# Kernel tuning notes

Hardware: AMD Instinct MI355X
Metric: run time of the kernel (lower is better)

## Reference

```python
import jax, jax.numpy as jnp
import numpy as np

DIM = 768
HEADS = 12
HEAD_DIM = DIM // HEADS
WS = 32                      # window_size (Wh == Ww)
N = WS * WS + 1              # tokens = patches + CLS
B = 8
NUM_REL = (2 * WS - 1) * (2 * WS - 1) + 3


def _rel_pos_index():
    # Mirrors the torch buffer construction (meshgrid indexing='ij').
    coords = np.stack(np.meshgrid(np.arange(WS), np.arange(WS), indexing='ij')).reshape(2, -1)
    rel = (coords[:, :, None] - coords[:, None, :]).transpose(1, 2, 0)  # [M, M, 2]
    rel[..., 0] += WS - 1
    rel[..., 1] += WS - 1
    rel[..., 0] *= 2 * WS - 1
    idx = np.zeros((N, N), dtype=np.int32)
    idx[1:, 1:] = rel.sum(-1)
    idx[0, :] = NUM_REL - 3
    idx[:, 0] = NUM_REL - 2
    idx[0, 0] = NUM_REL - 1
    return idx


def setup_inputs() -> dict:
    key = jax.random.key(0)
    ks = jax.random.split(key, 4)
    s = DIM ** -0.5
    return {
        "x": jax.random.normal(ks[0], (B, N, DIM), dtype=jnp.float32),
        "qkv_w": jax.random.normal(ks[1], (3 * DIM, DIM), dtype=jnp.float32) * s,
        "q_bias": jnp.zeros((DIM,), dtype=jnp.float32),
        "v_bias": jnp.zeros((DIM,), dtype=jnp.float32),
        "rpb_table": jax.random.normal(ks[2], (NUM_REL, HEADS), dtype=jnp.float32) * 0.02,
        "proj_w": jax.random.normal(ks[3], (DIM, DIM), dtype=jnp.float32) * s,
        "proj_b": jnp.zeros((DIM,), dtype=jnp.float32),
        "rel_pos_index": jnp.asarray(_rel_pos_index()),
    }


def reference(x, qkv_w, q_bias, v_bias, rpb_table, proj_w, proj_b, rel_pos_index):
    Bx, Nx, C = x.shape
    scale = HEAD_DIM ** -0.5
    # qkv bias = [q_bias, zeros, v_bias] (k has no bias)
    qkv_bias = jnp.concatenate([q_bias, jnp.zeros_like(v_bias), v_bias])
    qkv = x @ qkv_w.T + qkv_bias                           # [B, N, 3*C]
    qkv = qkv.reshape(Bx, Nx, 3, HEADS, HEAD_DIM).transpose(2, 0, 3, 1, 4)
    q, k, v = qkv[0] * scale, qkv[1], qkv[2]               # [B, H, N, d]
    attn = jnp.einsum('bhqd,bhkd->bhqk', q, k)             # [B, H, N, N]
    rpb = rpb_table[rel_pos_index]                         # [N, N, H] gather
    attn = attn + rpb.transpose(2, 0, 1)[None]             # broadcast over batch
    attn = jax.nn.softmax(attn, axis=-1)
    out = jnp.einsum('bhqk,bhkd->bhqd', attn, v)           # [B, H, N, d]
    out = out.transpose(0, 2, 1, 3).reshape(Bx, Nx, -1)    # [B, N, C]
    return out @ proj_w.T + proj_b
```

## Files before the change

kernel.cpp:

```cpp
#include <hip/hip_runtime.h>

typedef _Float16 f16;
typedef __attribute__((ext_vector_type(4))) _Float16 f16x4;
typedef __attribute__((ext_vector_type(8))) _Float16 f16x8;
typedef __attribute__((ext_vector_type(4))) float f32x4;

#define BATCH 8
#define NTOK 1025
#define DIM 768
#define HEADS 12
#define HD 64
#define MTOT (BATCH * NTOK)
#define MPAD 8320
#define NQP2 1152
#define NKP 1088
#define NUMREL 3972

#define DMA_FENCE asm volatile("s_waitcnt vmcnt(0)" ::: "memory")

__device__ __forceinline__ int imin(int a, int b) { return a < b ? a : b; }

__device__ __forceinline__ void gl_lds16(const f16* g, f16* l) {
  __builtin_amdgcn_global_load_lds(
      (const __attribute__((address_space(1))) unsigned int*)g,
      (__attribute__((address_space(3))) unsigned int*)l, 16, 0, 0);
}

__global__ __launch_bounds__(256) void cast3(const float* __restrict__ s0,
                                             f16* __restrict__ d0, int n0,
                                             const float* __restrict__ s1,
                                             f16* __restrict__ d1, int n1,
                                             const float* __restrict__ s2,
                                             f16* __restrict__ d2, int n2) {
  const float* s = (blockIdx.y == 0) ? s0 : (blockIdx.y == 1) ? s1 : s2;
  f16* d = (blockIdx.y == 0) ? d0 : (blockIdx.y == 1) ? d1 : d2;
  int n = (blockIdx.y == 0) ? n0 : (blockIdx.y == 1) ? n1 : n2;
  for (size_t i = ((size_t)blockIdx.x * 256 + threadIdx.x) * 8; i < (size_t)n;
       i += (size_t)gridDim.x * 256 * 8) {
    float4 a = *(const float4*)(s + i);
    float4 b = *(const float4*)(s + i + 4);
    f16x8 r;
    r[0] = (f16)a.x; r[1] = (f16)a.y; r[2] = (f16)a.z; r[3] = (f16)a.w;
    r[4] = (f16)b.x; r[5] = (f16)b.y; r[6] = (f16)b.z; r[7] = (f16)b.w;
    *(f16x8*)(d + i) = r;
  }
}

__device__ __forceinline__ float rpb_bias(const float* __restrict__ rpb, int qg,
                                          int kg, int h) {
  int idx;
  if (kg == 0) {
    idx = (qg == 0) ? (NUMREL - 1) : (NUMREL - 2);
  } else if (qg == 0) {
    idx = NUMREL - 3;
  } else {
    int qq = imin(qg, 1024) - 1, kk = imin(kg, 1024) - 1;
    int di = (qq >> 5) - (kk >> 5);
    int dj = (qq & 31) - (kk & 31);
    idx = (di + 31) * 63 + (dj + 31);
  }
  return rpb[idx * HEADS + h];
}

__global__ __launch_bounds__(256) void bias_pre(const float* __restrict__ rpb,
                                                f16* __restrict__ tbl) {
  const int kt = blockIdx.x / 17;
  const int qb17 = blockIdx.x % 17;
  const int h = blockIdx.y;
  const int tid = threadIdx.x;
  const int q = qb17 * 64 + (tid >> 2);
  const int lg = tid & 3;
  f16 vals[16];
#pragma unroll
  for (int c = 0; c < 4; c++)
#pragma unroll
    for (int r = 0; r < 4; r++) {
      int kv = kt * 64 + c * 16 + lg * 4 + r;
      float v = (kv >= NTOK) ? -30000.f : rpb_bias(rpb, q, kv, h);
      vals[c * 4 + r] = (f16)v;
    }
  size_t off = ((((size_t)h * 17 + kt) * NKP + q) * 4 + lg) * 16;
  *(f16x8*)(tbl + off) = *(const f16x8*)(&vals[0]);
  *(f16x8*)(tbl + off + 8) = *(const f16x8*)(&vals[8]);
}

__global__ __launch_bounds__(256) void qkv_gemm(
    const f16* __restrict__ Ah, const f16* __restrict__ Bh,
    const float* __restrict__ q_bias, const float* __restrict__ v_bias,
    f16* __restrict__ qb, f16* __restrict__ kb, f16* __restrict__ vtb) {
  __shared__ f16 As[2][128][64];
  __shared__ f16 Bs[2][128][64];
  const int tid = threadIdx.x;
  const int lane = tid & 63, w = tid >> 6;
  const int wm = w >> 1, wn = w & 1;
  const int lr = lane & 15, lg = lane >> 4;
  const int tN = blockIdx.x;
  const int tM = blockIdx.y;
  const int r8 = lane >> 3;
  const int swch = (lane & 7) ^ r8;
  const int lr7 = lr & 7;

  const f16* Ab = Ah + ((size_t)tM * 128 + r8) * DIM + swch * 8;
  const f16* Bb = Bh + ((size_t)tN * 128 + r8) * DIM + swch * 8;

#pragma unroll
  for (int pp = 0; pp < 4; pp++) {
    int rowb = w * 32 + pp * 8;
    gl_lds16(Ab + (size_t)rowb * DIM, &As[0][rowb][0]);
    gl_lds16(Bb + (size_t)rowb * DIM, &Bs[0][rowb][0]);
  }

  f32x4 acc[4][4] = {};

  for (int kt = 0; kt < 12; kt++) {
    const int bi = kt & 1;
    DMA_FENCE;
    __syncthreads();
    if (kt + 1 < 12) {
#pragma unroll
      for (int pp = 0; pp < 4; pp++) {
        int rowb = w * 32 + pp * 8;
        gl_lds16(Ab + (size_t)rowb * DIM + (kt + 1) * 64, &As[bi ^ 1][rowb][0]);
        gl_lds16(Bb + (size_t)rowb * DIM + (kt + 1) * 64, &Bs[bi ^ 1][rowb][0]);
      }
    }
#pragma unroll
    for (int ks = 0; ks < 2; ks++) {
      f16x8 af[4], bf[4];
      int rc = ((ks * 4 + lg) ^ lr7) * 8;
#pragma unroll
      for (int i = 0; i < 4; i++) {
        af[i] = *(const f16x8*)(&As[bi][wm * 64 + i * 16 + lr][rc]);
        bf[i] = *(const f16x8*)(&Bs[bi][wn * 64 + i * 16 + lr][rc]);
      }
#pragma unroll
      for (int mi = 0; mi < 4; mi++)
#pragma unroll
        for (int ni = 0; ni < 4; ni++)
          acc[mi][ni] = __builtin_amdgcn_mfma_f32_16x16x32_f16(
              af[mi], bf[ni], acc[mi][ni], 0, 0, 0);
    }
  }

  const int which = tN / 6;
  const int nb = tN % 6;
#pragma unroll
  for (int mi = 0; mi < 4; mi++) {
#pragma unroll
    for (int ni = 0; ni < 4; ni++) {
      int ncol = nb * 128 + wn * 64 + ni * 16 + lr;
      int h = ncol >> 6, dd = ncol & 63;
      float bias = 0.f;
      if (which == 0) bias = q_bias[ncol];
      if (which == 2) bias = v_bias[ncol];
#pragma unroll
      for (int r = 0; r < 4; r++) {
        int m = tM * 128 + wm * 64 + mi * 16 + lg * 4 + r;
        if (m >= MTOT) continue;
        int b = m / NTOK;
        int t = m - b * NTOK;
        int bh = b * HEADS + h;
        float v = acc[mi][ni][r] + bias;
        if (which == 0)
          qb[((size_t)bh * NQP2 + t) * HD + dd] = (f16)(v * 0.125f);
        else if (which == 1)
          kb[((size_t)bh * NKP + t) * HD + dd] = (f16)v;
        else
          vtb[((size_t)bh * HD + dd) * NKP + t] = (f16)v;
      }
    }
  }
}

__global__ __launch_bounds__(256) void attn_kernel(
    const f16* __restrict__ qb, const f16* __restrict__ kb,
    const f16* __restrict__ vtb, const f16* __restrict__ tbl,
    f16* __restrict__ ob) {
  __shared__ f16 Ks[2][64][64];
  __shared__ f16 Vs[2][64][64];
  __shared__ f16 Plds[4][16][72];
  const int tid = threadIdx.x;
  const int lane = tid & 63, w = tid >> 6;
  const int lr = lane & 15, lg = lane >> 4;
  const int b = blockIdx.x & 7;
  const int t9 = blockIdx.x >> 3;
  const int qblk = t9 % 9;
  const int h = t9 / 9;
  const int bh = b * HEADS + h;
  const int q0 = qblk * 128 + w * 32;

  const f16* kbase = kb + (size_t)bh * NKP * HD;
  const f16* vbase = vtb + (size_t)bh * HD * NKP;

  const int srow8 = lane >> 3;
  const int swch = (lane & 7) ^ srow8;

#pragma unroll
  for (int pp = 0; pp < 2; pp++) {
    int p = w * 2 + pp;
    int row = p * 8 + srow8;
    gl_lds16(kbase + (size_t)row * HD + swch * 8, &Ks[0][p * 8][0]);
    gl_lds16(vbase + (size_t)row * NKP + swch * 8, &Vs[0][p * 8][0]);
  }

  f16x8 aq[2][2];
#pragma unroll
  for (int g = 0; g < 2; g++) {
    const f16* qp = qb + ((size_t)bh * NQP2 + q0 + g * 16 + lr) * HD + lg * 8;
    aq[g][0] = *(const f16x8*)(qp);
    aq[g][1] = *(const f16x8*)(qp + 32);
  }

  const f16* bp[2];
#pragma unroll
  for (int g = 0; g < 2; g++) {
    int qt = imin(q0 + g * 16 + lr, NKP - 1);
    bp[g] = tbl + (((size_t)h * 17 * NKP + qt) * 4 + lg) * 16;
  }
  f16x8 bb[2][2];
#pragma unroll
  for (int g = 0; g < 2; g++) {
    bb[g][0] = *(const f16x8*)(bp[g]);
    bb[g][1] = *(const f16x8*)(bp[g] + 8);
  }

  float lsum[2] = {0.f, 0.f};
  f32x4 oacc[2][4] = {};
  const int sw8 = lr & 7;
  const size_t ktstride = (size_t)NKP * 64;

  for (int kt = 0; kt < 17; kt++) {
    const int bi = kt & 1;
    DMA_FENCE;
    __syncthreads();
    if (kt + 1 < 17) {
#pragma unroll
      for (int pp = 0; pp < 2; pp++) {
        int p = w * 2 + pp;
        int row = p * 8 + srow8;
        gl_lds16(kbase + (size_t)((kt + 1) * 64 + row) * HD + swch * 8,
                 &Ks[bi ^ 1][p * 8][0]);
        gl_lds16(vbase + (size_t)row * NKP + (kt + 1) * 64 + swch * 8,
                 &Vs[bi ^ 1][p * 8][0]);
      }
    }
    f16x8 nb[2][2] = {};
    if (kt + 1 < 17) {
#pragma unroll
      for (int g = 0; g < 2; g++) {
        const f16* p8 = bp[g] + (size_t)(kt + 1) * ktstride;
        nb[g][0] = *(const f16x8*)(p8);
        nb[g][1] = *(const f16x8*)(p8 + 8);
      }
    }
    f32x4 s[2][4];
#pragma unroll
    for (int g = 0; g < 2; g++)
#pragma unroll
      for (int c = 0; c < 4; c++) {
        const f16* src = (const f16*)&bb[g][c >> 1];
#pragma unroll
        for (int r = 0; r < 4; r++) s[g][c][r] = (float)src[(c & 1) * 4 + r];
      }
#pragma unroll
    for (int c = 0; c < 4; c++) {
      f16x8 kf0 = *(const f16x8*)(&Ks[bi][c * 16 + lr][(lg ^ sw8) * 8]);
      f16x8 kf1 = *(const f16x8*)(&Ks[bi][c * 16 + lr][((lg + 4) ^ sw8) * 8]);
      s[0][c] = __builtin_amdgcn_mfma_f32_16x16x32_f16(kf0, aq[0][0], s[0][c], 0, 0, 0);
      s[0][c] = __builtin_amdgcn_mfma_f32_16x16x32_f16(kf1, aq[0][1], s[0][c], 0, 0, 0);
      s[1][c] = __builtin_amdgcn_mfma_f32_16x16x32_f16(kf0, aq[1][0], s[1][c], 0, 0, 0);
      s[1][c] = __builtin_amdgcn_mfma_f32_16x16x32_f16(kf1, aq[1][1], s[1][c], 0, 0, 0);
    }
#pragma unroll
    for (int g = 0; g < 2; g++)
#pragma unroll
      for (int c = 0; c < 4; c++)
#pragma unroll
        for (int r = 0; r < 4; r++) {
          float p = __expf(s[g][c][r]);
          s[g][c][r] = p;
          lsum[g] += p;
        }
    f16x8 ap[2][2];
#pragma unroll
    for (int g = 0; g < 2; g++) {
#pragma unroll
      for (int c = 0; c < 4; c++) {
        f16x4 pk;
        pk[0] = (f16)s[g][c][0];
        pk[1] = (f16)s[g][c][1];
        pk[2] = (f16)s[g][c][2];
        pk[3] = (f16)s[g][c][3];
        *(f16x4*)(&Plds[w][lr][c * 16 + lg * 4]) = pk;
      }
      ap[g][0] = *(const f16x8*)(&Plds[w][lr][lg * 8]);
      ap[g][1] = *(const f16x8*)(&Plds[w][lr][32 + lg * 8]);
    }
#pragma unroll
    for (int dblk = 0; dblk < 4; dblk++) {
      f16x8 vf0 = *(const f16x8*)(&Vs[bi][dblk * 16 + lr][(lg ^ sw8) * 8]);
      f16x8 vf1 = *(const f16x8*)(&Vs[bi][dblk * 16 + lr][((lg + 4) ^ sw8) * 8]);
      oacc[0][dblk] = __builtin_amdgcn_mfma_f32_16x16x32_f16(ap[0][0], vf0, oacc[0][dblk], 0, 0, 0);
      oacc[0][dblk] = __builtin_amdgcn_mfma_f32_16x16x32_f16(ap[0][1], vf1, oacc[0][dblk], 0, 0, 0);
      oacc[1][dblk] = __builtin_amdgcn_mfma_f32_16x16x32_f16(ap[1][0], vf0, oacc[1][dblk], 0, 0, 0);
      oacc[1][dblk] = __builtin_amdgcn_mfma_f32_16x16x32_f16(ap[1][1], vf1, oacc[1][dblk], 0, 0, 0);
    }
#pragma unroll
    for (int g = 0; g < 2; g++) {
      bb[g][0] = nb[g][0];
      bb[g][1] = nb[g][1];
    }
  }
#pragma unroll
  for (int g = 0; g < 2; g++) {
    float ls = lsum[g];
    ls += __shfl_xor(ls, 16);
    ls += __shfl_xor(ls, 32);
    float inv[4];
#pragma unroll
    for (int r = 0; r < 4; r++) inv[r] = 1.f / __shfl(ls, lg * 4 + r);
#pragma unroll
    for (int dblk = 0; dblk < 4; dblk++)
#pragma unroll
      for (int r = 0; r < 4; r++) {
        int qg = q0 + g * 16 + lg * 4 + r;
        if (qg >= NTOK) continue;
        float v = oacc[g][dblk][r] * inv[r];
        ob[((size_t)(b * NTOK + qg)) * DIM + h * HD + dblk * 16 + lr] = (f16)v;
      }
  }
}

__global__ __launch_bounds__(256) void proj_gemm(const f16* __restrict__ Ah,
                                                 const f16* __restrict__ Bh,
                                                 const float* __restrict__ pb,
                                                 float* __restrict__ out) {
  __shared__ f16 As[2][128][64];
  __shared__ f16 Bs[2][128][64];
  const int tid = threadIdx.x;
  const int lane = tid & 63, w = tid >> 6;
  const int wm = w >> 1, wn = w & 1;
  const int lr = lane & 15, lg = lane >> 4;
  const int tN = blockIdx.x;
  const int tM = blockIdx.y;
  const int r8 = lane >> 3;
  const int swch = (lane & 7) ^ r8;
  const int lr7 = lr & 7;

  const f16* Ab = Ah + ((size_t)tM * 128 + r8) * DIM + swch * 8;
  const f16* Bb = Bh + ((size_t)tN * 128 + r8) * DIM + swch * 8;

#pragma unroll
  for (int pp = 0; pp < 4; pp++) {
    int rowb = w * 32 + pp * 8;
    gl_lds16(Ab + (size_t)rowb * DIM, &As[0][rowb][0]);
    gl_lds16(Bb + (size_t)rowb * DIM, &Bs[0][rowb][0]);
  }

  f32x4 acc[4][4] = {};

  for (int kt = 0; kt < 12; kt++) {
    const int bi = kt & 1;
    DMA_FENCE;
    __syncthreads();
    if (kt + 1 < 12) {
#pragma unroll
      for (int pp = 0; pp < 4; pp++) {
        int rowb = w * 32 + pp * 8;
        gl_lds16(Ab + (size_t)rowb * DIM + (kt + 1) * 64, &As[bi ^ 1][rowb][0]);
        gl_lds16(Bb + (size_t)rowb * DIM + (kt + 1) * 64, &Bs[bi ^ 1][rowb][0]);
      }
    }
#pragma unroll
    for (int ks = 0; ks < 2; ks++) {
      f16x8 af[4], bf[4];
      int rc = ((ks * 4 + lg) ^ lr7) * 8;
#pragma unroll
      for (int i = 0; i < 4; i++) {
        af[i] = *(const f16x8*)(&As[bi][wm * 64 + i * 16 + lr][rc]);
        bf[i] = *(const f16x8*)(&Bs[bi][wn * 64 + i * 16 + lr][rc]);
      }
#pragma unroll
      for (int mi = 0; mi < 4; mi++)
#pragma unroll
        for (int ni = 0; ni < 4; ni++)
          acc[mi][ni] = __builtin_amdgcn_mfma_f32_16x16x32_f16(
              af[mi], bf[ni], acc[mi][ni], 0, 0, 0);
    }
  }

#pragma unroll
  for (int mi = 0; mi < 4; mi++) {
#pragma unroll
    for (int ni = 0; ni < 4; ni++) {
      int n = tN * 128 + wn * 64 + ni * 16 + lr;
      float bias = pb[n];
#pragma unroll
      for (int r = 0; r < 4; r++) {
        int m = tM * 128 + wm * 64 + mi * 16 + lg * 4 + r;
        if (m >= MTOT) continue;
        out[(size_t)m * DIM + n] = acc[mi][ni][r] + bias;
      }
    }
  }
}

extern "C" void kernel_launch(void* const* d_in, const int* in_sizes, int n_in,
                              void* d_out, int out_size, void* d_ws,
                              size_t ws_size, hipStream_t stream) {
  const float* x = (const float*)d_in[0];
  const float* qkv_w = (const float*)d_in[1];
  const float* q_bias = (const float*)d_in[2];
  const float* v_bias = (const float*)d_in[3];
  const float* rpb = (const float*)d_in[4];
  const float* proj_w = (const float*)d_in[5];
  const float* proj_b = (const float*)d_in[6];
  float* out = (float*)d_out;

  f16* xh = (f16*)d_ws;
  f16* wh = xh + (size_t)MPAD * DIM;
  f16* pwh = wh + (size_t)3 * DIM * DIM;
  f16* qb = pwh + (size_t)DIM * DIM;
  f16* kb = qb + (size_t)BATCH * HEADS * NQP2 * HD;
  f16* vtb = kb + (size_t)BATCH * HEADS * NKP * HD;
  f16* ob = vtb + (size_t)BATCH * HEADS * NKP * HD;
  f16* tbl = ob + (size_t)MPAD * DIM;

  cast3<<<dim3(1024, 3), 256, 0, stream>>>(
      x, xh, MTOT * DIM, qkv_w, wh, 3 * DIM * DIM, proj_w, pwh, DIM * DIM);
  bias_pre<<<dim3(17 * 17, HEADS), 256, 0, stream>>>(rpb, tbl);
  qkv_gemm<<<dim3(18, 65), 256, 0, stream>>>(xh, wh, q_bias, v_bias, qb, kb,
                                             vtb);
  attn_kernel<<<dim3(BATCH * HEADS * 9), 256, 0, stream>>>(qb, kb, vtb, tbl,
                                                           ob);
  proj_gemm<<<dim3(6, 65), 256, 0, stream>>>(ob, pwh, proj_b, out);
}
```

Before: 294.6 us.

## Replace double-buffered LDS prefetch with single-buffer load-then-compute in GEMMs

Both the QKV and projection GEMM kernels drop their double-buffered shared-memory pipeline. They now load one K tile, wait, compute, and sync again before the next load. This halves LDS use per block, which may allow more resident blocks per CU. In exchange, the overlap between global loads and MFMA compute within a block is lost, and each iteration adds an extra barrier.

```diff
diff --git a/kernel.cpp b/kernel.cpp
--- a/kernel.cpp
+++ b/kernel.cpp
@@ -88,8 +88,8 @@
     const f16* __restrict__ Ah, const f16* __restrict__ Bh,
     const float* __restrict__ q_bias, const float* __restrict__ v_bias,
     f16* __restrict__ qb, f16* __restrict__ kb, f16* __restrict__ vtb) {
-  __shared__ f16 As[2][128][64];
-  __shared__ f16 Bs[2][128][64];
+  __shared__ f16 As[128][64];
+  __shared__ f16 Bs[128][64];
   const int tid = threadIdx.x;
   const int lane = tid & 63, w = tid >> 6;
   const int wm = w >> 1, wn = w & 1;
@@ -103,35 +103,25 @@
   const f16* Ab = Ah + ((size_t)tM * 128 + r8) * DIM + swch * 8;
   const f16* Bb = Bh + ((size_t)tN * 128 + r8) * DIM + swch * 8;
 
-#pragma unroll
-  for (int pp = 0; pp < 4; pp++) {
-    int rowb = w * 32 + pp * 8;
-    gl_lds16(Ab + (size_t)rowb * DIM, &As[0][rowb][0]);
-    gl_lds16(Bb + (size_t)rowb * DIM, &Bs[0][rowb][0]);
-  }
-
   f32x4 acc[4][4] = {};
 
   for (int kt = 0; kt < 12; kt++) {
-    const int bi = kt & 1;
+#pragma unroll
+    for (int pp = 0; pp < 4; pp++) {
+      int rowb = w * 32 + pp * 8;
+      gl_lds16(Ab + (size_t)rowb * DIM + kt * 64, &As[rowb][0]);
+      gl_lds16(Bb + (size_t)rowb * DIM + kt * 64, &Bs[rowb][0]);
+    }
     DMA_FENCE;
     __syncthreads();
-    if (kt + 1 < 12) {
-#pragma unroll
-      for (int pp = 0; pp < 4; pp++) {
-        int rowb = w * 32 + pp * 8;
-        gl_lds16(Ab + (size_t)rowb * DIM + (kt + 1) * 64, &As[bi ^ 1][rowb][0]);
-        gl_lds16(Bb + (size_t)rowb * DIM + (kt + 1) * 64, &Bs[bi ^ 1][rowb][0]);
-      }
-    }
 #pragma unroll
     for (int ks = 0; ks < 2; ks++) {
       f16x8 af[4], bf[4];
       int rc = ((ks * 4 + lg) ^ lr7) * 8;
 #pragma unroll
       for (int i = 0; i < 4; i++) {
-        af[i] = *(const f16x8*)(&As[bi][wm * 64 + i * 16 + lr][rc]);
-        bf[i] = *(const f16x8*)(&Bs[bi][wn * 64 + i * 16 + lr][rc]);
+        af[i] = *(const f16x8*)(&As[wm * 64 + i * 16 + lr][rc]);
+        bf[i] = *(const f16x8*)(&Bs[wn * 64 + i * 16 + lr][rc]);
       }
 #pragma unroll
       for (int mi = 0; mi < 4; mi++)
@@ -140,6 +130,7 @@
           acc[mi][ni] = __builtin_amdgcn_mfma_f32_16x16x32_f16(
               af[mi], bf[ni], acc[mi][ni], 0, 0, 0);
     }
+    __syncthreads();
   }
 
   const int which = tN / 6;
@@ -335,8 +326,8 @@
                                                  const f16* __restrict__ Bh,
                                                  const float* __restrict__ pb,
                                                  float* __restrict__ out) {
-  __shared__ f16 As[2][128][64];
-  __shared__ f16 Bs[2][128][64];
+  __shared__ f16 As[128][64];
+  __shared__ f16 Bs[128][64];
   const int tid = threadIdx.x;
   const int lane = tid & 63, w = tid >> 6;
   const int wm = w >> 1, wn = w & 1;
@@ -350,35 +341,25 @@
   const f16* Ab = Ah + ((size_t)tM * 128 + r8) * DIM + swch * 8;
   const f16* Bb = Bh + ((size_t)tN * 128 + r8) * DIM + swch * 8;
 
-#pragma unroll
-  for (int pp = 0; pp < 4; pp++) {
-    int rowb = w * 32 + pp * 8;
-    gl_lds16(Ab + (size_t)rowb * DIM, &As[0][rowb][0]);
-    gl_lds16(Bb + (size_t)rowb * DIM, &Bs[0][rowb][0]);
-  }
-
   f32x4 acc[4][4] = {};
 
   for (int kt = 0; kt < 12; kt++) {
-    const int bi = kt & 1;
+#pragma unroll
+    for (int pp = 0; pp < 4; pp++) {
+      int rowb = w * 32 + pp * 8;
+      gl_lds16(Ab + (size_t)rowb * DIM + kt * 64, &As[rowb][0]);
+      gl_lds16(Bb + (size_t)rowb * DIM + kt * 64, &Bs[rowb][0]);
+    }
     DMA_FENCE;
     __syncthreads();
-    if (kt + 1 < 12) {
-#pragma unroll
-      for (int pp = 0; pp < 4; pp++) {
-        int rowb = w * 32 + pp * 8;
-        gl_lds16(Ab + (size_t)rowb * DIM + (kt + 1) * 64, &As[bi ^ 1][rowb][0]);
-        gl_lds16(Bb + (size_t)rowb * DIM + (kt + 1) * 64, &Bs[bi ^ 1][rowb][0]);
-      }
-    }
 #pragma unroll
     for (int ks = 0; ks < 2; ks++) {
       f16x8 af[4], bf[4];
       int rc = ((ks * 4 + lg) ^ lr7) * 8;
 #pragma unroll
       for (int i = 0; i < 4; i++) {
-        af[i] = *(const f16x8*)(&As[bi][wm * 64 + i * 16 + lr][rc]);
-        bf[i] = *(const f16x8*)(&Bs[bi][wn * 64 + i * 16 + lr][rc]);
+        af[i] = *(const f16x8*)(&As[wm * 64 + i * 16 + lr][rc]);
+        bf[i] = *(const f16x8*)(&Bs[wn * 64 + i * 16 + lr][rc]);
       }
 #pragma unroll
       for (int mi = 0; mi < 4; mi++)
@@ -387,6 +368,7 @@
           acc[mi][ni] = __builtin_amdgcn_mfma_f32_16x16x32_f16(
               af[mi], bf[ni], acc[mi][ni], 0, 0, 0);
     }
+    __syncthreads();
   }
 
 #pragma unroll
```

Result: no change. 295.4 us (+0.3%).
